# Kernel tuning notes

Hardware: AMD Instinct MI355X
Metric: run time of the kernel (lower is better)

The kernel has to match this reference:

```python
import jax, jax.numpy as jnp
import numpy as np

EPS = 1e-6
HEADS, HEAD_DIM = 8, 64

def rms_norm_ch(x, g):
    # x: [B,C,H,W], normalize over channel dim, scale g: [C]
    mean = jnp.mean(x * x, axis=1, keepdims=True)
    return x * jax.lax.rsqrt(mean + EPS) * g[None, :, None, None]

def rms_norm_last(x, g):
    # x: [B,L,D], normalize over feature dim, scale g: [D]
    mean = jnp.mean(x * x, axis=-1, keepdims=True)
    return x * jax.lax.rsqrt(mean + EPS) * g

def setup_inputs() -> dict:
    key = jax.random.key(0)
    ks = jax.random.split(key, 5)
    B, C, H, W = 8, 512, 32, 32
    Lc = 1024
    hidden = HEADS * HEAD_DIM  # 512
    x = jax.random.normal(ks[0], (B, C, H, W), dtype=jnp.float32)
    context = jax.random.normal(ks[1], (B, Lc, C), dtype=jnp.float32)
    Wq = jax.random.normal(ks[2], (hidden, C), dtype=jnp.float32) * 0.02
    Wkv = jax.random.normal(ks[3], (2 * hidden, C), dtype=jnp.float32) * 0.02
    Wo = jax.random.normal(ks[4], (C, hidden), dtype=jnp.float32) * 0.02
    bo = jnp.zeros((C,), dtype=jnp.float32)
    g = jnp.ones((C,), dtype=jnp.float32)   # shared RMSNorm scale (pre-attn)
    g2 = jnp.ones((C,), dtype=jnp.float32)  # output RMSNorm scale
    return {"x": x, "context": context, "Wq": Wq, "Wkv": Wkv, "Wo": Wo, "bo": bo, "g": g, "g2": g2}

def reference(x, context, Wq, Wkv, Wo, bo, g, g2):
    B, C, H, W = x.shape
    Lc = context.shape[1]
    hidden = HEADS * HEAD_DIM
    scale = HEAD_DIM ** -0.5

    # Q projection: 1x1 conv == per-pixel matmul
    xn = rms_norm_ch(x, g)
    q = jnp.einsum('oc,bchw->bohw', Wq, xn)                     # [B,hidden,H,W]
    q = q.reshape(B, HEADS, HEAD_DIM, H * W) * scale            # [B,h,d,lw1]

    # K,V from context tokens
    cn = rms_norm_last(context, g)
    kv = jnp.einsum('bld,od->blo', cn, Wkv)                     # [B,Lc,2*hidden]
    k, v = jnp.split(kv, 2, axis=-1)
    k = k.reshape(B, Lc, HEADS, HEAD_DIM).transpose(0, 2, 3, 1)  # [B,h,d,lw2]
    v = v.reshape(B, Lc, HEADS, HEAD_DIM).transpose(0, 2, 3, 1)  # [B,h,d,lw2]

    sim = jnp.einsum('bhci,bhcj->bhij', q, k)                   # [B,h,lw1,lw2]
    attn = jax.nn.softmax(sim, axis=-1)
    out = jnp.einsum('bhij,bhcj->bhic', attn, v)                # [B,h,lw1,d]

    out = out.transpose(0, 1, 3, 2).reshape(B, hidden, H, W)    # b (h c) l w
    y = jnp.einsum('oc,bchw->bohw', Wo, out) + bo[None, :, None, None]
    y = rms_norm_ch(y, g2)
    return y + x
```

## Files before the change

kernel.cpp:

```cpp
#include <hip/hip_runtime.h>
#include <hip/hip_bf16.h>

using bf16 = __hip_bfloat16;
typedef float f32x4 __attribute__((ext_vector_type(4)));
typedef short s16x8 __attribute__((ext_vector_type(8)));
typedef short s16x4 __attribute__((ext_vector_type(4)));

#define B_N   8
#define C_N   512
#define HW_N  1024
#define LC_N  1024
#define HID_N 512
#define NHEAD 8
#define DHEAD 64
#define EPSN  1e-6f

__device__ __forceinline__ f32x4 mfma16(s16x8 a, s16x8 b, f32x4 c) {
  return __builtin_amdgcn_mfma_f32_16x16x32_bf16(a, b, c, 0, 0, 0);
}
__device__ __forceinline__ void gload_lds16(const void* g, void* l) {
  __builtin_amdgcn_global_load_lds((const __attribute__((address_space(1))) void*)g,
                                   (__attribute__((address_space(3))) void*)l, 16, 0, 0);
}
__device__ __forceinline__ s16x8 ld8(const bf16* p) {
  return *reinterpret_cast<const s16x8*>(p);
}
__device__ __forceinline__ unsigned short bfbits(float f) {
  return __builtin_bit_cast(unsigned short, __float2bfloat16(f));
}

__global__ __launch_bounds__(256) void prep_weights(
    const float* __restrict__ Wq, const float* __restrict__ Wkv,
    const float* __restrict__ Wo, const float* __restrict__ g,
    bf16* __restrict__ Wqg, bf16* __restrict__ Wkvg, bf16* __restrict__ Wob)
{
  int idx = blockIdx.x * 256 + threadIdx.x;
  const int NQ = 512 * 512, NKV = 1024 * 512;
  if (idx < NQ) {
    Wqg[idx] = __float2bfloat16(Wq[idx] * g[idx & 511]);
  } else if (idx < NQ + NKV) {
    int j = idx - NQ;
    Wkvg[j] = __float2bfloat16(Wkv[j] * g[j & 511]);
  } else {
    int j = idx - NQ - NKV;
    Wob[j] = __float2bfloat16(Wo[j]);
  }
}

__global__ __launch_bounds__(256) void rstd_ch_kernel(
    const float* __restrict__ x, float* __restrict__ rstd)
{
  __shared__ float part[4][64];
  int tp = threadIdx.x & 63, tc = threadIdx.x >> 6;
  int gp = blockIdx.x * 64 + tp;
  int b = gp >> 10, p = gp & 1023;
  const float* xb = x + (long)b * C_N * HW_N + p;
  float s = 0.f;
  for (int c = tc * 128; c < tc * 128 + 128; ++c) {
    float v = xb[(long)c * HW_N];
    s += v * v;
  }
  part[tc][tp] = s;
  __syncthreads();
  if (tc == 0) {
    float tot = part[0][tp] + part[1][tp] + part[2][tp] + part[3][tp];
    rstd[gp] = rsqrtf(tot * (1.0f / C_N) + EPSN);
  }
}

__global__ __launch_bounds__(256) void xbf_kernel(
    const float* __restrict__ x, const float* __restrict__ rstd, bf16* __restrict__ xbf)
{
  __shared__ float tile[32][33];
  int b = blockIdx.z, c0 = blockIdx.y * 32, p0 = blockIdx.x * 32;
  int tx = threadIdx.x & 31, ty = threadIdx.x >> 5;
#pragma unroll
  for (int j = 0; j < 4; ++j) {
    int c = ty + j * 8;
    tile[c][tx] = x[((long)b * C_N + c0 + c) * HW_N + p0 + tx];
  }
  __syncthreads();
#pragma unroll
  for (int j = 0; j < 4; ++j) {
    int p = ty + j * 8;
    float r = rstd[b * HW_N + p0 + p];
    xbf[((long)b * HW_N + p0 + p) * C_N + c0 + tx] = __float2bfloat16(tile[tx][p] * r);
  }
}

__global__ __launch_bounds__(256) void ctxnorm_kernel(
    const float* __restrict__ ctx, bf16* __restrict__ cnbf)
{
  int row = blockIdx.x * 4 + (threadIdx.x >> 6);
  int lane = threadIdx.x & 63;
  const float* cr = ctx + (long)row * C_N;
  float4 v0 = ((const float4*)cr)[lane * 2];
  float4 v1 = ((const float4*)cr)[lane * 2 + 1];
  float s = v0.x*v0.x + v0.y*v0.y + v0.z*v0.z + v0.w*v0.w
          + v1.x*v1.x + v1.y*v1.y + v1.z*v1.z + v1.w*v1.w;
#pragma unroll
  for (int m = 1; m < 64; m <<= 1) s += __shfl_xor(s, m);
  float r = rsqrtf(s * (1.0f / C_N) + EPSN);
  bf16 tmp[8];
  tmp[0] = __float2bfloat16(v0.x * r); tmp[1] = __float2bfloat16(v0.y * r);
  tmp[2] = __float2bfloat16(v0.z * r); tmp[3] = __float2bfloat16(v0.w * r);
  tmp[4] = __float2bfloat16(v1.x * r); tmp[5] = __float2bfloat16(v1.y * r);
  tmp[6] = __float2bfloat16(v1.z * r); tmp[7] = __float2bfloat16(v1.w * r);
  *reinterpret_cast<s16x8*>(cnbf + (long)row * C_N + lane * 8) =
      *reinterpret_cast<const s16x8*>(tmp);
}

template<int MODE>
__global__ __launch_bounds__(256, 4)
void gemm_nt(const bf16* __restrict__ A, const bf16* __restrict__ W,
             void* __restrict__ outp, bf16* __restrict__ vT,
             int N, int K, float scale)
{
  __shared__ bf16 sA[2][128 * 32];
  __shared__ bf16 sB[2][64 * 32];
  const int t = threadIdx.x;
  const int m0 = blockIdx.x * 128;
  const int n0 = blockIdx.y * 64;
  const int lane = t & 63;
  const int w = t >> 6;
  const int wm = w * 32;
  const int lr = lane & 15, hi = lane >> 4;
  const int r = t >> 2, seg = t & 3;

  const long aoff0 = (long)(m0 + r) * K + seg * 8;
  const long aoff1 = (long)(m0 + 64 + r) * K + seg * 8;
  const long woff  = (long)(n0 + r) * K + seg * 8;
  const int ld8i = t * 8;

  f32x4 acc[2][4] = {};

#define GSTAGE(buf, k0)                                    \
  do {                                                     \
    gload_lds16(A + aoff0 + (k0), &sA[buf][ld8i]);         \
    gload_lds16(A + aoff1 + (k0), &sA[buf][2048 + ld8i]);  \
    gload_lds16(W + woff  + (k0), &sB[buf][ld8i]);         \
  } while (0)

  GSTAGE(0, 0);
  __syncthreads();
  int cur = 0;
  for (int k0 = 0; k0 < K; k0 += 32) {
    if (k0 + 32 < K) GSTAGE(cur ^ 1, k0 + 32);
    s16x8 af[2], bfr[4];
#pragma unroll
    for (int mi = 0; mi < 2; ++mi)
      af[mi] = *reinterpret_cast<const s16x8*>(&sA[cur][(wm + mi * 16 + lr) * 32 + hi * 8]);
#pragma unroll
    for (int ni = 0; ni < 4; ++ni)
      bfr[ni] = *reinterpret_cast<const s16x8*>(&sB[cur][(ni * 16 + lr) * 32 + hi * 8]);
#pragma unroll
    for (int mi = 0; mi < 2; ++mi)
#pragma unroll
      for (int ni = 0; ni < 4; ++ni)
        acc[mi][ni] = mfma16(af[mi], bfr[ni], acc[mi][ni]);
    __syncthreads();
    cur ^= 1;
  }
#undef GSTAGE

#pragma unroll
  for (int mi = 0; mi < 2; ++mi) {
#pragma unroll
    for (int ni = 0; ni < 4; ++ni) {
#pragma unroll
      for (int rr = 0; rr < 4; ++rr) {
        int row = m0 + wm + mi * 16 + hi * 4 + rr;
        int col = n0 + ni * 16 + lr;
        float v = acc[mi][ni][rr] * scale;
        if (MODE == 2) {
          ((float*)outp)[(long)row * N + col] = v;
        } else if (MODE == 0) {
          ((bf16*)outp)[(long)row * N + col] = __float2bfloat16(v);
        } else {
          if (col < HID_N) {
            ((bf16*)outp)[(long)row * N + col] = __float2bfloat16(v);
          } else {
            int b = row >> 10, l = row & 1023;
            vT[((long)b * HID_N + (col - HID_N)) * LC_N + l] = __float2bfloat16(v);
          }
        }
      }
    }
  }
}

__global__ __launch_bounds__(256, 2)
void attn_fused(const bf16* __restrict__ qbf, const bf16* __restrict__ kvbf,
                const bf16* __restrict__ vT, bf16* __restrict__ attno)
{
  __shared__ bf16 sK[2][4096];
  __shared__ bf16 sV[2][4096];
  __shared__ bf16 Pl[4][32 * 72];
  const int t = threadIdx.x;
  const int wv = t >> 6, lane = t & 63;
  const int lr = lane & 15, hi = lane >> 4;
  const int hi8 = hi * 8, hi4 = hi * 4;
  const int bh = blockIdx.x, b = bh >> 3, h = bh & 7;
  const int q_base = blockIdx.y * 128 + wv * 32;

  const bf16* kbase = kvbf + (long)b * LC_N * 1024 + h * DHEAD;
  const bf16* vbase = vT + ((long)b * HID_N + h * DHEAD) * (long)LC_N;
  bf16* Pw = Pl[wv];

  s16x8 qf[2][2];
#pragma unroll
  for (int qt = 0; qt < 2; ++qt)
#pragma unroll
    for (int c = 0; c < 2; ++c)
      qf[qt][c] = ld8(qbf + ((long)b * HW_N + q_base + qt * 16 + lr) * HID_N
                          + h * DHEAD + c * 32 + hi8);

  const int srow = lane >> 2;
  const int scol = (lane & 3) * 8;

#define ASTAGE(buf, l0n)                                                        \
  do {                                                                          \
    _Pragma("unroll")                                                           \
    for (int j = 0; j < 4; ++j) {                                               \
      int lin = wv * 4 + j;                                                     \
      int cc = (lin >> 2) & 1, qq = lin & 3;                                    \
      if (lin < 8) {                                                            \
        gload_lds16(kbase + (long)((l0n) + qq * 16 + srow) * 1024 + cc * 32 + scol, \
                    &sK[buf][cc * 2048 + qq * 512 + lane * 8]);                 \
      } else {                                                                  \
        gload_lds16(vbase + (long)(qq * 16 + srow) * 1024 + (l0n) + cc * 32 + scol, \
                    &sV[buf][cc * 2048 + qq * 512 + lane * 8]);                 \
      }                                                                         \
    }                                                                           \
  } while (0)

  float m[2] = {-1e30f, -1e30f};
  float lsum[2] = {0.f, 0.f};
  f32x4 o[2][4] = {};

  ASTAGE(0, 0);
  __syncthreads();
  int cur = 0;

#pragma unroll 1
  for (int l0 = 0; l0 < LC_N; l0 += 64) {
    if (l0 + 64 < LC_N) ASTAGE(cur ^ 1, l0 + 64);

    f32x4 st[4][2] = {};
#pragma unroll
    for (int kt = 0; kt < 4; ++kt) {
      s16x8 k0 = *reinterpret_cast<const s16x8*>(&sK[cur][(kt * 16 + lr) * 32 + hi8]);
      s16x8 k1 = *reinterpret_cast<const s16x8*>(&sK[cur][2048 + (kt * 16 + lr) * 32 + hi8]);
      st[kt][0] = mfma16(k0, qf[0][0], st[kt][0]);
      st[kt][0] = mfma16(k1, qf[0][1], st[kt][0]);
      st[kt][1] = mfma16(k0, qf[1][0], st[kt][1]);
      st[kt][1] = mfma16(k1, qf[1][1], st[kt][1]);
    }

    float pmax[2];
#pragma unroll
    for (int qt = 0; qt < 2; ++qt) {
      float mx = st[0][qt][0];
#pragma unroll
      for (int kt = 0; kt < 4; ++kt)
#pragma unroll
        for (int rr = 0; rr < 4; ++rr)
          mx = fmaxf(mx, st[kt][qt][rr]);
      pmax[qt] = mx;
    }
    bool ok = (pmax[0] <= m[0] + 8.f) && (pmax[1] <= m[1] + 8.f);
    if (!__all(ok)) {
#pragma unroll
      for (int qt = 0; qt < 2; ++qt) {
        float rm = pmax[qt];
        rm = fmaxf(rm, __shfl_xor(rm, 16));
        rm = fmaxf(rm, __shfl_xor(rm, 32));
        float mn = fmaxf(m[qt], rm);
        float al = __builtin_amdgcn_exp2f(m[qt] - mn);
        m[qt] = mn;
        lsum[qt] *= al;
        float arr[4];
#pragma unroll
        for (int rr = 0; rr < 4; ++rr) arr[rr] = __shfl(al, hi4 + rr);
#pragma unroll
        for (int dt = 0; dt < 4; ++dt)
#pragma unroll
          for (int rr = 0; rr < 4; ++rr) o[qt][dt][rr] *= arr[rr];
      }
    }

#pragma unroll
    for (int qt = 0; qt < 2; ++qt) {
      float ls = 0.f;
#pragma unroll
      for (int kt = 0; kt < 4; ++kt) {
        float p0 = __builtin_amdgcn_exp2f(st[kt][qt][0] - m[qt]);
        float p1 = __builtin_amdgcn_exp2f(st[kt][qt][1] - m[qt]);
        float p2 = __builtin_amdgcn_exp2f(st[kt][qt][2] - m[qt]);
        float p3 = __builtin_amdgcn_exp2f(st[kt][qt][3] - m[qt]);
        ls += (p0 + p1) + (p2 + p3);
        s16x4 pk;
        pk[0] = (short)bfbits(p0); pk[1] = (short)bfbits(p1);
        pk[2] = (short)bfbits(p2); pk[3] = (short)bfbits(p3);
        *reinterpret_cast<s16x4*>(&Pw[(qt * 16 + lr) * 72 + kt * 16 + hi4]) = pk;
      }
      lsum[qt] += ls;
    }

#pragma unroll
    for (int c = 0; c < 2; ++c) {
      s16x8 pa0 = *reinterpret_cast<const s16x8*>(&Pw[(0 * 16 + lr) * 72 + c * 32 + hi8]);
      s16x8 pa1 = *reinterpret_cast<const s16x8*>(&Pw[(1 * 16 + lr) * 72 + c * 32 + hi8]);
#pragma unroll
      for (int dt = 0; dt < 4; ++dt) {
        s16x8 vv = *reinterpret_cast<const s16x8*>(
            &sV[cur][c * 2048 + (dt * 16 + lr) * 32 + hi8]);
        o[0][dt] = mfma16(pa0, vv, o[0][dt]);
        o[1][dt] = mfma16(pa1, vv, o[1][dt]);
      }
    }

    __syncthreads();
    cur ^= 1;
  }
#undef ASTAGE

#pragma unroll
  for (int qt = 0; qt < 2; ++qt) {
    float ls = lsum[qt];
    ls += __shfl_xor(ls, 16);
    ls += __shfl_xor(ls, 32);
    float linv[4];
#pragma unroll
    for (int rr = 0; rr < 4; ++rr) linv[rr] = 1.f / __shfl(ls, hi4 + rr);
#pragma unroll
    for (int dt = 0; dt < 4; ++dt)
#pragma unroll
      for (int rr = 0; rr < 4; ++rr)
        attno[((long)b * HW_N + q_base + qt * 16 + hi4 + rr) * HID_N
              + h * DHEAD + dt * 16 + lr] = __float2bfloat16(o[qt][dt][rr] * linv[rr]);
  }
}

__global__ __launch_bounds__(256) void ystats_kernel(
    const float* __restrict__ ytmp, const float* __restrict__ bo, float* __restrict__ rstdy)
{
  int row = blockIdx.x * 4 + (threadIdx.x >> 6);
  int lane = threadIdx.x & 63;
  const float* yr = ytmp + (long)row * C_N;
  float s = 0.f;
#pragma unroll
  for (int j = 0; j < 2; ++j) {
    float4 v = ((const float4*)yr)[lane * 2 + j];
    float4 bb = ((const float4*)bo)[lane * 2 + j];
    v.x += bb.x; v.y += bb.y; v.z += bb.z; v.w += bb.w;
    s += v.x*v.x + v.y*v.y + v.z*v.z + v.w*v.w;
  }
#pragma unroll
  for (int m = 1; m < 64; m <<= 1) s += __shfl_xor(s, m);
  rstdy[row] = rsqrtf(s * (1.0f / C_N) + EPSN);
}

__global__ __launch_bounds__(256) void final_kernel(
    const float* __restrict__ ytmp, const float* __restrict__ bo,
    const float* __restrict__ g2, const float* __restrict__ rstdy,
    const float* __restrict__ x, float* __restrict__ out)
{
  __shared__ float tile[32][33];
  int b = blockIdx.z, c0 = blockIdx.y * 32, p0 = blockIdx.x * 32;
  int tx = threadIdx.x & 31, ty = threadIdx.x >> 5;
#pragma unroll
  for (int j = 0; j < 4; ++j) {
    int p = ty + j * 8;
    tile[p][tx] = ytmp[((long)b * HW_N + p0 + p) * C_N + c0 + tx] + bo[c0 + tx];
  }
  __syncthreads();
#pragma unroll
  for (int j = 0; j < 4; ++j) {
    int c = ty + j * 8;
    long oidx = ((long)b * C_N + c0 + c) * HW_N + p0 + tx;
    out[oidx] = tile[tx][c] * rstdy[b * HW_N + p0 + tx] * g2[c0 + c] + x[oidx];
  }
}

extern "C" void kernel_launch(void* const* d_in, const int* in_sizes, int n_in,
                              void* d_out, int out_size, void* d_ws, size_t ws_size,
                              hipStream_t stream) {
  const float* x   = (const float*)d_in[0];
  const float* ctx = (const float*)d_in[1];
  const float* Wq  = (const float*)d_in[2];
  const float* Wkv = (const float*)d_in[3];
  const float* Wo  = (const float*)d_in[4];
  const float* bo  = (const float*)d_in[5];
  const float* g   = (const float*)d_in[6];
  const float* g2  = (const float*)d_in[7];
  float* out = (float*)d_out;

  char* ws = (char*)d_ws;
  bf16*  Wqg   = (bf16*)(ws + 0);
  bf16*  Wkvg  = (bf16*)(ws + 524288);
  bf16*  Wob   = (bf16*)(ws + 1572864);
  float* rstdx = (float*)(ws + 2097152);
  float* rstdy = (float*)(ws + 2129920);
  bf16*  xbf   = (bf16*)(ws + 2162688);
  bf16*  cnbf  = (bf16*)(ws + 10551296);
  bf16*  qbf   = (bf16*)(ws + 18939904);
  bf16*  kvbf  = (bf16*)(ws + 27328512);
  bf16*  vT    = (bf16*)(ws + 44105728);
  bf16*  attno = (bf16*)(ws + 52494336);
  float* ytmp  = (float*)(ws + 2162688);

  prep_weights<<<4096, 256, 0, stream>>>(Wq, Wkv, Wo, g, Wqg, Wkvg, Wob);
  rstd_ch_kernel<<<128, 256, 0, stream>>>(x, rstdx);
  xbf_kernel<<<dim3(32, 16, 8), 256, 0, stream>>>(x, rstdx, xbf);
  ctxnorm_kernel<<<2048, 256, 0, stream>>>(ctx, cnbf);

  gemm_nt<0><<<dim3(64, 8), 256, 0, stream>>>(
      xbf, Wqg, qbf, nullptr, HID_N, C_N, 0.18033688011112042f);
  gemm_nt<1><<<dim3(64, 16), 256, 0, stream>>>(
      cnbf, Wkvg, kvbf, vT, 2 * HID_N, C_N, 1.0f);

  attn_fused<<<dim3(64, 8), 256, 0, stream>>>(qbf, kvbf, vT, attno);

  gemm_nt<2><<<dim3(64, 8), 256, 0, stream>>>(
      attno, Wob, ytmp, nullptr, C_N, HID_N, 1.0f);

  ystats_kernel<<<2048, 256, 0, stream>>>(ytmp, bo, rstdy);
  final_kernel<<<dim3(32, 16, 8), 256, 0, stream>>>(ytmp, bo, g2, rstdy, x, out);
}
```

Measured before the change: 192.6 us.

## Merge Q/KV GEMMs, enlarge GEMM tiles, fuse output RMS stats via atomics

Replaces the templated 128x64 GEMM with a 128x128 tile core and launches the Q and KV projections as a single grid. The output projection epilogue now adds the bias and accumulates per-row sum of squares with atomics, which removes the separate ystats pass and the re-read of ytmp. The rstd_ch kernel is split across more blocks for parallelism, and the ssq buffer is zeroed inside prep_weights. Larger tiles raise register pressure (occupancy bound 2), and atomics make the reduction order nondeterministic.

```diff
diff --git a/kernel.cpp b/kernel.cpp
--- a/kernel.cpp
+++ b/kernel.cpp
@@ -32,10 +32,12 @@
 __global__ __launch_bounds__(256) void prep_weights(
     const float* __restrict__ Wq, const float* __restrict__ Wkv,
     const float* __restrict__ Wo, const float* __restrict__ g,
-    bf16* __restrict__ Wqg, bf16* __restrict__ Wkvg, bf16* __restrict__ Wob)
+    bf16* __restrict__ Wqg, bf16* __restrict__ Wkvg, bf16* __restrict__ Wob,
+    float* __restrict__ ssq)
 {
   int idx = blockIdx.x * 256 + threadIdx.x;
   const int NQ = 512 * 512, NKV = 1024 * 512;
+  if (idx < 8192) ssq[idx] = 0.f;
   if (idx < NQ) {
     Wqg[idx] = __float2bfloat16(Wq[idx] * g[idx & 511]);
   } else if (idx < NQ + NKV) {
@@ -50,20 +52,22 @@
 __global__ __launch_bounds__(256) void rstd_ch_kernel(
     const float* __restrict__ x, float* __restrict__ rstd)
 {
-  __shared__ float part[4][64];
-  int tp = threadIdx.x & 63, tc = threadIdx.x >> 6;
-  int gp = blockIdx.x * 64 + tp;
+  __shared__ float part[16][16];
+  int tp = threadIdx.x & 15, tc = threadIdx.x >> 4;
+  int gp = blockIdx.x * 16 + tp;
   int b = gp >> 10, p = gp & 1023;
   const float* xb = x + (long)b * C_N * HW_N + p;
   float s = 0.f;
-  for (int c = tc * 128; c < tc * 128 + 128; ++c) {
+  for (int c = tc * 32; c < tc * 32 + 32; ++c) {
     float v = xb[(long)c * HW_N];
     s += v * v;
   }
   part[tc][tp] = s;
   __syncthreads();
   if (tc == 0) {
-    float tot = part[0][tp] + part[1][tp] + part[2][tp] + part[3][tp];
+    float tot = 0.f;
+#pragma unroll
+    for (int i = 0; i < 16; ++i) tot += part[i][tp];
     rstd[gp] = rsqrtf(tot * (1.0f / C_N) + EPSN);
   }
 }
@@ -110,35 +114,27 @@
       *reinterpret_cast<const s16x8*>(tmp);
 }
 
-template<int MODE>
-__global__ __launch_bounds__(256, 4)
-void gemm_nt(const bf16* __restrict__ A, const bf16* __restrict__ W,
-             void* __restrict__ outp, bf16* __restrict__ vT,
-             int N, int K, float scale)
-{
-  __shared__ bf16 sA[2][128 * 32];
-  __shared__ bf16 sB[2][64 * 32];
+__device__ __forceinline__ void gemm128_core(
+    const bf16* __restrict__ A, const bf16* __restrict__ W, int K, int m0, int n0,
+    bf16* __restrict__ sA, bf16* __restrict__ sB, f32x4 (&acc)[4][4])
+{
   const int t = threadIdx.x;
-  const int m0 = blockIdx.x * 128;
-  const int n0 = blockIdx.y * 64;
-  const int lane = t & 63;
-  const int w = t >> 6;
-  const int wm = w * 32;
+  const int lane = t & 63, w = t >> 6;
+  const int wm = (w >> 1) * 64, wn = (w & 1) * 64;
   const int lr = lane & 15, hi = lane >> 4;
   const int r = t >> 2, seg = t & 3;
-
   const long aoff0 = (long)(m0 + r) * K + seg * 8;
   const long aoff1 = (long)(m0 + 64 + r) * K + seg * 8;
-  const long woff  = (long)(n0 + r) * K + seg * 8;
-  const int ld8i = t * 8;
-
-  f32x4 acc[2][4] = {};
-
-#define GSTAGE(buf, k0)                                    \
-  do {                                                     \
-    gload_lds16(A + aoff0 + (k0), &sA[buf][ld8i]);         \
-    gload_lds16(A + aoff1 + (k0), &sA[buf][2048 + ld8i]);  \
-    gload_lds16(W + woff  + (k0), &sB[buf][ld8i]);         \
+  const long woff0 = (long)(n0 + r) * K + seg * 8;
+  const long woff1 = (long)(n0 + 64 + r) * K + seg * 8;
+  const int d0 = r * 32 + seg * 8, d1 = (64 + r) * 32 + seg * 8;
+
+#define GSTAGE(buf, k0)                                           \
+  do {                                                            \
+    gload_lds16(A + aoff0 + (k0), &sA[(buf) * 4096 + d0]);        \
+    gload_lds16(A + aoff1 + (k0), &sA[(buf) * 4096 + d1]);        \
+    gload_lds16(W + woff0 + (k0), &sB[(buf) * 4096 + d0]);        \
+    gload_lds16(W + woff1 + (k0), &sB[(buf) * 4096 + d1]);        \
   } while (0)
 
   GSTAGE(0, 0);
@@ -146,15 +142,17 @@
   int cur = 0;
   for (int k0 = 0; k0 < K; k0 += 32) {
     if (k0 + 32 < K) GSTAGE(cur ^ 1, k0 + 32);
-    s16x8 af[2], bfr[4];
-#pragma unroll
-    for (int mi = 0; mi < 2; ++mi)
-      af[mi] = *reinterpret_cast<const s16x8*>(&sA[cur][(wm + mi * 16 + lr) * 32 + hi * 8]);
+    s16x8 af[4], bfr[4];
+#pragma unroll
+    for (int mi = 0; mi < 4; ++mi)
+      af[mi] = *reinterpret_cast<const s16x8*>(
+          &sA[cur * 4096 + (wm + mi * 16 + lr) * 32 + hi * 8]);
 #pragma unroll
     for (int ni = 0; ni < 4; ++ni)
-      bfr[ni] = *reinterpret_cast<const s16x8*>(&sB[cur][(ni * 16 + lr) * 32 + hi * 8]);
-#pragma unroll
-    for (int mi = 0; mi < 2; ++mi)
+      bfr[ni] = *reinterpret_cast<const s16x8*>(
+          &sB[cur * 4096 + (wn + ni * 16 + lr) * 32 + hi * 8]);
+#pragma unroll
+    for (int mi = 0; mi < 4; ++mi)
 #pragma unroll
       for (int ni = 0; ni < 4; ++ni)
         acc[mi][ni] = mfma16(af[mi], bfr[ni], acc[mi][ni]);
@@ -162,31 +160,101 @@
     cur ^= 1;
   }
 #undef GSTAGE
-
-#pragma unroll
-  for (int mi = 0; mi < 2; ++mi) {
+}
+
+__global__ __launch_bounds__(256, 2)
+void gemm_qkv(const bf16* __restrict__ xbf, const bf16* __restrict__ cnbf,
+              const bf16* __restrict__ Wqg, const bf16* __restrict__ Wkvg,
+              bf16* __restrict__ qbf, bf16* __restrict__ kvbf, bf16* __restrict__ vT)
+{
+  __shared__ bf16 sA[2 * 4096];
+  __shared__ bf16 sB[2 * 4096];
+  const int bid = blockIdx.x;
+  const bf16 *A, *W;
+  int N, m0, n0;
+  bool isQ;
+  if (bid < 256) {
+    isQ = true;  A = xbf;  W = Wqg;  N = HID_N;
+    m0 = (bid >> 2) * 128; n0 = (bid & 3) * 128;
+  } else {
+    isQ = false; A = cnbf; W = Wkvg; N = 2 * HID_N;
+    int b2 = bid - 256;
+    m0 = (b2 >> 3) * 128; n0 = (b2 & 7) * 128;
+  }
+  f32x4 acc[4][4] = {};
+  gemm128_core(A, W, C_N, m0, n0, sA, sB, acc);
+
+  const int lane = threadIdx.x & 63, w = threadIdx.x >> 6;
+  const int wm = (w >> 1) * 64, wn = (w & 1) * 64;
+  const int lr = lane & 15, hi = lane >> 4;
+  const float scale = isQ ? 0.18033688011112042f : 1.0f;
+#pragma unroll
+  for (int mi = 0; mi < 4; ++mi) {
 #pragma unroll
     for (int ni = 0; ni < 4; ++ni) {
 #pragma unroll
       for (int rr = 0; rr < 4; ++rr) {
         int row = m0 + wm + mi * 16 + hi * 4 + rr;
-        int col = n0 + ni * 16 + lr;
+        int col = n0 + wn + ni * 16 + lr;
         float v = acc[mi][ni][rr] * scale;
-        if (MODE == 2) {
-          ((float*)outp)[(long)row * N + col] = v;
-        } else if (MODE == 0) {
-          ((bf16*)outp)[(long)row * N + col] = __float2bfloat16(v);
+        if (isQ) {
+          qbf[(long)row * HID_N + col] = __float2bfloat16(v);
+        } else if (col < HID_N) {
+          kvbf[(long)row * (2 * HID_N) + col] = __float2bfloat16(v);
         } else {
-          if (col < HID_N) {
-            ((bf16*)outp)[(long)row * N + col] = __float2bfloat16(v);
-          } else {
-            int b = row >> 10, l = row & 1023;
-            vT[((long)b * HID_N + (col - HID_N)) * LC_N + l] = __float2bfloat16(v);
-          }
+          int b = row >> 10, l = row & 1023;
+          vT[((long)b * HID_N + (col - HID_N)) * LC_N + l] = __float2bfloat16(v);
         }
       }
     }
   }
+}
+
+__global__ __launch_bounds__(256, 2)
+void gemm_o(const bf16* __restrict__ attno, const bf16* __restrict__ Wob,
+            const float* __restrict__ bo, float* __restrict__ ytmp,
+            float* __restrict__ ssq)
+{
+  __shared__ bf16 sA[2 * 4096];
+  __shared__ bf16 sB[2 * 4096];
+  const int m0 = (blockIdx.x >> 2) * 128;
+  const int n0 = (blockIdx.x & 3) * 128;
+  f32x4 acc[4][4] = {};
+  gemm128_core(attno, Wob, HID_N, m0, n0, sA, sB, acc);
+
+  const int lane = threadIdx.x & 63, w = threadIdx.x >> 6;
+  const int wm = (w >> 1) * 64, wn = (w & 1) * 64;
+  const int lr = lane & 15, hi = lane >> 4;
+  float ss[4][4];
+#pragma unroll
+  for (int mi = 0; mi < 4; ++mi)
+#pragma unroll
+    for (int rr = 0; rr < 4; ++rr) ss[mi][rr] = 0.f;
+
+#pragma unroll
+  for (int mi = 0; mi < 4; ++mi) {
+#pragma unroll
+    for (int ni = 0; ni < 4; ++ni) {
+      float bb = bo[n0 + wn + ni * 16 + lr];
+#pragma unroll
+      for (int rr = 0; rr < 4; ++rr) {
+        int row = m0 + wm + mi * 16 + hi * 4 + rr;
+        int col = n0 + wn + ni * 16 + lr;
+        float v = acc[mi][ni][rr] + bb;
+        ytmp[(long)row * C_N + col] = v;
+        ss[mi][rr] += v * v;
+      }
+    }
+  }
+#pragma unroll
+  for (int mi = 0; mi < 4; ++mi)
+#pragma unroll
+    for (int rr = 0; rr < 4; ++rr) {
+      float s = ss[mi][rr];
+      s += __shfl_xor(s, 1); s += __shfl_xor(s, 2);
+      s += __shfl_xor(s, 4); s += __shfl_xor(s, 8);
+      if (lr == 0) atomicAdd(&ssq[m0 + wm + mi * 16 + hi * 4 + rr], s);
+    }
 }
 
 __global__ __launch_bounds__(256, 2)
@@ -342,29 +410,10 @@
   }
 }
 
-__global__ __launch_bounds__(256) void ystats_kernel(
-    const float* __restrict__ ytmp, const float* __restrict__ bo, float* __restrict__ rstdy)
-{
-  int row = blockIdx.x * 4 + (threadIdx.x >> 6);
-  int lane = threadIdx.x & 63;
-  const float* yr = ytmp + (long)row * C_N;
-  float s = 0.f;
-#pragma unroll
-  for (int j = 0; j < 2; ++j) {
-    float4 v = ((const float4*)yr)[lane * 2 + j];
-    float4 bb = ((const float4*)bo)[lane * 2 + j];
-    v.x += bb.x; v.y += bb.y; v.z += bb.z; v.w += bb.w;
-    s += v.x*v.x + v.y*v.y + v.z*v.z + v.w*v.w;
-  }
-#pragma unroll
-  for (int m = 1; m < 64; m <<= 1) s += __shfl_xor(s, m);
-  rstdy[row] = rsqrtf(s * (1.0f / C_N) + EPSN);
-}
-
 __global__ __launch_bounds__(256) void final_kernel(
-    const float* __restrict__ ytmp, const float* __restrict__ bo,
-    const float* __restrict__ g2, const float* __restrict__ rstdy,
-    const float* __restrict__ x, float* __restrict__ out)
+    const float* __restrict__ ytmp, const float* __restrict__ g2,
+    const float* __restrict__ ssq, const float* __restrict__ x,
+    float* __restrict__ out)
 {
   __shared__ float tile[32][33];
   int b = blockIdx.z, c0 = blockIdx.y * 32, p0 = blockIdx.x * 32;
@@ -372,14 +421,15 @@
 #pragma unroll
   for (int j = 0; j < 4; ++j) {
     int p = ty + j * 8;
-    tile[p][tx] = ytmp[((long)b * HW_N + p0 + p) * C_N + c0 + tx] + bo[c0 + tx];
+    tile[p][tx] = ytmp[((long)b * HW_N + p0 + p) * C_N + c0 + tx];
   }
   __syncthreads();
+  float r = rsqrtf(ssq[b * HW_N + p0 + tx] * (1.0f / C_N) + EPSN);
 #pragma unroll
   for (int j = 0; j < 4; ++j) {
     int c = ty + j * 8;
     long oidx = ((long)b * C_N + c0 + c) * HW_N + p0 + tx;
-    out[oidx] = tile[tx][c] * rstdy[b * HW_N + p0 + tx] * g2[c0 + c] + x[oidx];
+    out[oidx] = tile[tx][c] * r * g2[c0 + c] + x[oidx];
   }
 }
 
@@ -401,7 +451,7 @@
   bf16*  Wkvg  = (bf16*)(ws + 524288);
   bf16*  Wob   = (bf16*)(ws + 1572864);
   float* rstdx = (float*)(ws + 2097152);
-  float* rstdy = (float*)(ws + 2129920);
+  float* ssq   = (float*)(ws + 2129920);
   bf16*  xbf   = (bf16*)(ws + 2162688);
   bf16*  cnbf  = (bf16*)(ws + 10551296);
   bf16*  qbf   = (bf16*)(ws + 18939904);
@@ -410,21 +460,16 @@
   bf16*  attno = (bf16*)(ws + 52494336);
   float* ytmp  = (float*)(ws + 2162688);
 
-  prep_weights<<<4096, 256, 0, stream>>>(Wq, Wkv, Wo, g, Wqg, Wkvg, Wob);
-  rstd_ch_kernel<<<128, 256, 0, stream>>>(x, rstdx);
+  prep_weights<<<4096, 256, 0, stream>>>(Wq, Wkv, Wo, g, Wqg, Wkvg, Wob, ssq);
+  rstd_ch_kernel<<<512, 256, 0, stream>>>(x, rstdx);
   xbf_kernel<<<dim3(32, 16, 8), 256, 0, stream>>>(x, rstdx, xbf);
   ctxnorm_kernel<<<2048, 256, 0, stream>>>(ctx, cnbf);
 
-  gemm_nt<0><<<dim3(64, 8), 256, 0, stream>>>(
-      xbf, Wqg, qbf, nullptr, HID_N, C_N, 0.18033688011112042f);
-  gemm_nt<1><<<dim3(64, 16), 256, 0, stream>>>(
-      cnbf, Wkvg, kvbf, vT, 2 * HID_N, C_N, 1.0f);
+  gemm_qkv<<<768, 256, 0, stream>>>(xbf, cnbf, Wqg, Wkvg, qbf, kvbf, vT);
 
   attn_fused<<<dim3(64, 8), 256, 0, stream>>>(qbf, kvbf, vT, attno);
 
-  gemm_nt<2><<<dim3(64, 8), 256, 0, stream>>>(
-      attno, Wob, ytmp, nullptr, C_N, HID_N, 1.0f);
-
-  ystats_kernel<<<2048, 256, 0, stream>>>(ytmp, bo, rstdy);
-  final_kernel<<<dim3(32, 16, 8), 256, 0, stream>>>(ytmp, bo, g2, rstdy, x, out);
-}
+  gemm_o<<<256, 256, 0, stream>>>(attno, Wob, bo, ytmp, ssq);
+
+  final_kernel<<<dim3(32, 16, 8), 256, 0, stream>>>(ytmp, g2, ssq, x, out);
+}
```

Result: no change. 193.3 us (+0.4%).
